# Optimization experiments

Measured on AMD Instinct MI355X. Metric: run time of the kernel, lower is better.

The kernel has to match this reference:

```python
import jax, jax.numpy as jnp
import numpy as np

EPS = 1e-6  # AbsMeanFunction eps
LN_EPS = 1e-5


def _absmean_core(W):
    # gamma = mean(|W|) + eps; quantize to {-1, 0, +1}
    gamma = jnp.mean(jnp.abs(W)) + EPS
    Ws = W / gamma
    Wq = jnp.sign(Ws) * jnp.minimum(jnp.round(jnp.abs(Ws)), 1.0)
    return Wq, gamma


@jax.custom_vjp
def absmean(W):
    return _absmean_core(W)[0]


def _absmean_fwd(W):
    Wq, gamma = _absmean_core(W)
    return Wq, gamma


def _absmean_bwd(gamma, g):
    # custom backward from AbsMeanFunction: grad_W = grad_output / gamma
    return (g / gamma,)


absmean.defvjp(_absmean_fwd, _absmean_bwd)


def layernorm(x, w, b, eps=LN_EPS):
    mu = jnp.mean(x, axis=-1, keepdims=True)
    var = jnp.mean((x - mu) ** 2, axis=-1, keepdims=True)
    return (x - mu) * jax.lax.rsqrt(var + eps) * w + b


def setup_inputs() -> dict:
    key = jax.random.key(0)
    k1, k2, k3 = jax.random.split(key, 3)
    d, h = 1024, 4096  # n_embd, mlp_factor * n_embd
    B, T = 8, 2048
    return {
        "x": jax.random.normal(k1, (B, T, d), jnp.float32),
        "W_fc": jax.random.normal(k2, (h, d), jnp.float32),   # BitLinear158 weight (out, in)
        "ln_w": jnp.ones((h,), jnp.float32),
        "ln_b": jnp.zeros((h,), jnp.float32),
        "W_proj": jax.random.normal(k3, (d, h), jnp.float32),  # BitLinear158 weight (out, in)
    }


def reference(x, W_fc, ln_w, ln_b, W_proj):
    # c_fc: ternary-quantized linear, no bias
    h = jnp.einsum('btd,hd->bth', x, absmean(W_fc))
    # exact (erf) GELU matches torch nn.GELU default
    h = jax.nn.gelu(h, approximate=False)
    h = layernorm(h, ln_w, ln_b)
    # c_proj: ternary-quantized linear, no bias; dropout p=0 is identity
    return jnp.einsum('bth,dh->btd', h, absmean(W_proj))
```

## Files before the change

kernel.cpp:

```cpp
#include <hip/hip_runtime.h>
#include <hip/hip_bf16.h>

typedef __attribute__((ext_vector_type(8))) short bf16x8;
typedef __attribute__((ext_vector_type(4))) float f32x4;
typedef unsigned short u16;

#define D_IN  1024
#define D_HID 4096
#define MROWS 16384

__device__ __forceinline__ float b2f(u16 u) {
    union { unsigned int i; float f; } c; c.i = ((unsigned int)u) << 16; return c.f;
}
__device__ __forceinline__ u16 f2b(float f) {
    unsigned int u = __builtin_bit_cast(unsigned int, f);
    return (u16)((u + 0x7FFFu + ((u >> 16) & 1u)) >> 16);
}

__device__ __forceinline__ float gelu_fast(float v) {
    float p = v * fmaf(0.044715f * v, v, 1.0f);
    float e = __builtin_amdgcn_exp2f(-2.302202983f * p);
    return v * __builtin_amdgcn_rcpf(1.0f + e);
}

__device__ __forceinline__ float rowsum16(float v) {
    int t;
    t = __builtin_amdgcn_update_dpp(0, __builtin_bit_cast(int, v), 0x111, 0xf, 0xf, true);
    v += __builtin_bit_cast(float, t);
    t = __builtin_amdgcn_update_dpp(0, __builtin_bit_cast(int, v), 0x112, 0xf, 0xf, true);
    v += __builtin_bit_cast(float, t);
    t = __builtin_amdgcn_update_dpp(0, __builtin_bit_cast(int, v), 0x114, 0xf, 0xf, true);
    v += __builtin_bit_cast(float, t);
    t = __builtin_amdgcn_update_dpp(0, __builtin_bit_cast(int, v), 0x118, 0xf, 0xf, true);
    v += __builtin_bit_cast(float, t);
    return v;
}

__global__ void prep1(const float* __restrict__ x, const float* __restrict__ W0,
                      const float* __restrict__ W1, u16* __restrict__ xb,
                      float* __restrict__ partials, int n4, int n8) {
    const int y = blockIdx.y;
    if (y == 2) {
        const int stride = gridDim.x * blockDim.x;
        for (int i = blockIdx.x * blockDim.x + threadIdx.x; i < n8; i += stride) {
            float4 a = ((const float4*)x)[2 * i];
            float4 c = ((const float4*)x)[2 * i + 1];
            bf16x8 o;
            o[0] = (short)f2b(a.x); o[1] = (short)f2b(a.y); o[2] = (short)f2b(a.z); o[3] = (short)f2b(a.w);
            o[4] = (short)f2b(c.x); o[5] = (short)f2b(c.y); o[6] = (short)f2b(c.z); o[7] = (short)f2b(c.w);
            ((bf16x8*)xb)[i] = o;
        }
        return;
    }
    const float* W = y ? W1 : W0;
    float* out = partials + y * 1024;
    __shared__ float sdata[256];
    float s = 0.f;
    const int stride = gridDim.x * blockDim.x;
    for (int i = blockIdx.x * blockDim.x + threadIdx.x; i < n4; i += stride) {
        float4 v = ((const float4*)W)[i];
        s += fabsf(v.x) + fabsf(v.y) + fabsf(v.z) + fabsf(v.w);
    }
    sdata[threadIdx.x] = s;
    __syncthreads();
    for (int off = 128; off > 0; off >>= 1) {
        if (threadIdx.x < off) sdata[threadIdx.x] += sdata[threadIdx.x + off];
        __syncthreads();
    }
    if (threadIdx.x == 0) out[blockIdx.x] = sdata[0];
}

__global__ void absmean_finalize2(const float* __restrict__ partials, float inv_n,
                                  float* __restrict__ gamma) {
    const float* p = partials + blockIdx.x * 1024;
    __shared__ float sdata[256];
    float s = 0.f;
    for (int i = threadIdx.x; i < 1024; i += 256) s += p[i];
    sdata[threadIdx.x] = s;
    __syncthreads();
    for (int off = 128; off > 0; off >>= 1) {
        if (threadIdx.x < off) sdata[threadIdx.x] += sdata[threadIdx.x + off];
        __syncthreads();
    }
    if (threadIdx.x == 0) gamma[blockIdx.x] = sdata[0] * inv_n + 1e-6f;
}

__global__ void prep2(const float* __restrict__ W0, const float* __restrict__ W1,
                      const float* __restrict__ lnw, const float* __restrict__ lnb,
                      const float* __restrict__ gamma,
                      u16* __restrict__ Q0, u16* __restrict__ Q1,
                      float* __restrict__ c1, float* __restrict__ c0, int n4) {
    const int y = blockIdx.y;
    if (y == 2) {
        const float thr = 0.5f * gamma[1];
        const float* row = W1 + (size_t)blockIdx.x * D_HID;
        float s1 = 0.f, s0 = 0.f;
        for (int h = threadIdx.x; h < D_HID; h += 256) {
            float v = row[h];
            float t = v > thr ? 1.f : (v < -thr ? -1.f : 0.f);
            s1 += lnw[h] * t;
            s0 += lnb[h] * t;
        }
#pragma unroll
        for (int off = 32; off > 0; off >>= 1) {
            s1 += __shfl_down(s1, off);
            s0 += __shfl_down(s0, off);
        }
        __shared__ float sh1[4], sh0[4];
        const int wave = threadIdx.x >> 6, lane = threadIdx.x & 63;
        if (lane == 0) { sh1[wave] = s1; sh0[wave] = s0; }
        __syncthreads();
        if (threadIdx.x == 0) {
            c1[blockIdx.x] = sh1[0] + sh1[1] + sh1[2] + sh1[3];
            c0[blockIdx.x] = sh0[0] + sh0[1] + sh0[2] + sh0[3];
        }
        return;
    }
    const float* W = y ? W1 : W0;
    u16* Wq = y ? Q1 : Q0;
    const float thr = 0.5f * gamma[y];
    const int stride = gridDim.x * blockDim.x;
    for (int i = blockIdx.x * blockDim.x + threadIdx.x; i < n4; i += stride) {
        float4 v = ((const float4*)W)[i];
        ushort4 q;
        if (y == 0) {
            q.x = v.x > thr ? 0x3F80u : (v.x < -thr ? 0xBF80u : 0u);
            q.y = v.y > thr ? 0x3F80u : (v.y < -thr ? 0xBF80u : 0u);
            q.z = v.z > thr ? 0x3F80u : (v.z < -thr ? 0xBF80u : 0u);
            q.w = v.w > thr ? 0x3F80u : (v.w < -thr ? 0xBF80u : 0u);
        } else {
            const int h = (i * 4) & (D_HID - 1);
            float w0 = lnw[h], w1 = lnw[h + 1], w2 = lnw[h + 2], w3 = lnw[h + 3];
            q.x = v.x > thr ? f2b(w0) : (v.x < -thr ? f2b(-w0) : 0u);
            q.y = v.y > thr ? f2b(w1) : (v.y < -thr ? f2b(-w1) : 0u);
            q.z = v.z > thr ? f2b(w2) : (v.z < -thr ? f2b(-w2) : 0u);
            q.w = v.w > thr ? f2b(w3) : (v.w < -thr ? f2b(-w3) : 0u);
        }
        ((ushort4*)Wq)[i] = q;
    }
}

template <int EPI>
__global__ __launch_bounds__(512, 2)
void gemm256(const u16* __restrict__ A, const u16* __restrict__ B,
             void* __restrict__ Cout, int M, int N, int K, int nbx,
             float* __restrict__ pS, float* __restrict__ pSS,
             const float* __restrict__ c1t, const float* __restrict__ c0t)
{
    (void)M;
    __shared__ u16 lds[65536];
    char* const ldsc = (char*)lds;
    const int tid = threadIdx.x;
    const int w = tid >> 6, lane = tid & 63;

    const int nwg = (int)gridDim.x;
    const int qq = nwg >> 3;
    const int bid = (int)blockIdx.x;
    const int swz = (bid & 7) * qq + (bid >> 3);
    const int bx = swz % nbx, by = swz / nbx;
    const size_t m0 = (size_t)by * 256, n0 = (size_t)bx * 256;

    const int wm = (w >> 2) * 128;
    const int wn = (w & 3) * 64;

    const int d0 = tid * 16;
    const int rrow = (d0 >> 6) & 15;
    const int sr0 = ((d0 >> 11) & 3) * 16 + rrow;
    const int cbx = (d0 & 63) ^ (((rrow >> 3) & 1) << 5);
    const int gc  = ((d0 >> 10) & 1) * 32 + (cbx >> 1);

    const int laneoffsw = (((lane & 15) * 64) + ((lane >> 4) * 16)) ^ (((lane >> 3) & 1) << 5);
    const int aoff = ((wm >> 7) << 14) + laneoffsw;
    const int boff = 65536 + ((wn >> 7) << 14) + (((wn >> 4) & 7) << 11) + laneoffsw;

    f32x4 acc[8][4];
#pragma unroll
    for (int i = 0; i < 8; ++i)
#pragma unroll
        for (int j = 0; j < 4; ++j) acc[i][j] = (f32x4){0.f, 0.f, 0.f, 0.f};

    bf16x8 a[4][2], b[4][2];

#define STAGE_A(KT, BUFB, HH) do {                                                              \
    const u16* _s = A + (size_t)(m0 + (HH) * 128 + sr0) * K + (size_t)(KT) * 64 + gc;           \
    __builtin_amdgcn_global_load_lds((const __attribute__((address_space(1))) void*)_s,         \
        (__attribute__((address_space(3))) void*)(ldsc + (BUFB) * 32768 + (HH) * 16384 + w * 1024), 16, 0, 0); \
    __builtin_amdgcn_global_load_lds((const __attribute__((address_space(1))) void*)(_s + (size_t)64 * K), \
        (__attribute__((address_space(3))) void*)(ldsc + (BUFB) * 32768 + (HH) * 16384 + w * 1024 + 8192), 16, 0, 0); \
} while (0)

#define STAGE_B(KT, BUFB, HH) do {                                                              \
    const u16* _s = B + (size_t)(n0 + (HH) * 128 + sr0) * K + (size_t)(KT) * 64 + gc;           \
    __builtin_amdgcn_global_load_lds((const __attribute__((address_space(1))) void*)_s,         \
        (__attribute__((address_space(3))) void*)(ldsc + 65536 + (BUFB) * 32768 + (HH) * 16384 + w * 1024), 16, 0, 0); \
    __builtin_amdgcn_global_load_lds((const __attribute__((address_space(1))) void*)(_s + (size_t)64 * K), \
        (__attribute__((address_space(3))) void*)(ldsc + 65536 + (BUFB) * 32768 + (HH) * 16384 + w * 1024 + 8192), 16, 0, 0); \
} while (0)

#define RD_A(BUFB, S, KS) (*(const bf16x8*)(ldsc + (BUFB) * 32768 + aoff + ((S) << 11) + ((KS) << 10)))
#define RD_B(BUFB, S, KS) (*(const bf16x8*)(ldsc + (BUFB) * 32768 + boff + ((S) << 11) + ((KS) << 10)))

#define MM(MB, NB) do {                                                                         \
    _Pragma("unroll") for (int ii = 0; ii < 4; ++ii)                                            \
    _Pragma("unroll") for (int jj = 0; jj < 2; ++jj)                                            \
    _Pragma("unroll") for (int kk = 0; kk < 2; ++kk)                                            \
        acc[(MB) + ii][(NB) + jj] = __builtin_amdgcn_mfma_f32_16x16x32_bf16(                    \
            a[ii][kk], b[(NB) + jj][kk], acc[(MB) + ii][(NB) + jj], 0, 0, 0);                   \
} while (0)

#define BARR()  asm volatile("s_barrier" ::: "memory")
#define LGKM0() asm volatile("s_waitcnt lgkmcnt(0)" ::: "memory")

#define ITER(F) do {                                                                            \
    _Pragma("unroll") for (int s = 0; s < 4; ++s) { a[s][0] = RD_A(0, s, 0); a[s][1] = RD_A(0, s, 1); } \
    _Pragma("unroll") for (int s = 0; s < 2; ++s) { b[s][0] = RD_B(0, s, 0); b[s][1] = RD_B(0, s, 1); } \
    STAGE_A(t + 1, 1, 0);                                                                       \
    asm volatile("s_waitcnt lgkmcnt(8)" ::: "memory");                                          \
    BARR(); LGKM0();                                                                            \
    __builtin_amdgcn_s_setprio(1); MM(0, 0); __builtin_amdgcn_s_setprio(0); BARR();             \
    _Pragma("unroll") for (int s = 2; s < 4; ++s) { b[s][0] = RD_B(0, s, 0); b[s][1] = RD_B(0, s, 1); } \
    STAGE_A(t + 1, 1, 1);                                                                       \
    BARR(); LGKM0();                                                                            \
    __builtin_amdgcn_s_setprio(1); MM(0, 2); __builtin_amdgcn_s_setprio(0); BARR();             \
    _Pragma("unroll") for (int s = 0; s < 4; ++s) { a[s][0] = RD_A(0, 4 + s, 0); a[s][1] = RD_A(0, 4 + s, 1); } \
    if (F) STAGE_B(t + 2, 0, 0);                                                                \
    BARR(); LGKM0();                                                                            \
    __builtin_amdgcn_s_setprio(1); MM(4, 0); __builtin_amdgcn_s_setprio(0); BARR();             \
    if (F) { STAGE_B(t + 2, 0, 1); asm volatile("s_waitcnt vmcnt(4)" ::: "memory"); }           \
    else   { asm volatile("s_waitcnt vmcnt(0)" ::: "memory"); }                                 \
    BARR();                                                                                     \
    __builtin_amdgcn_s_setprio(1); MM(4, 2); __builtin_amdgcn_s_setprio(0); BARR();             \
    _Pragma("unroll") for (int s = 0; s < 4; ++s) { a[s][0] = RD_A(1, s, 0); a[s][1] = RD_A(1, s, 1); } \
    _Pragma("unroll") for (int s = 0; s < 2; ++s) { b[s][0] = RD_B(1, s, 0); b[s][1] = RD_B(1, s, 1); } \
    if (F) STAGE_A(t + 2, 0, 0);                                                                \
    asm volatile("s_waitcnt lgkmcnt(8)" ::: "memory");                                          \
    BARR(); LGKM0();                                                                            \
    __builtin_amdgcn_s_setprio(1); MM(0, 0); __builtin_amdgcn_s_setprio(0); BARR();             \
    _Pragma("unroll") for (int s = 2; s < 4; ++s) { b[s][0] = RD_B(1, s, 0); b[s][1] = RD_B(1, s, 1); } \
    if (F) STAGE_A(t + 2, 0, 1);                                                                \
    BARR(); LGKM0();                                                                            \
    __builtin_amdgcn_s_setprio(1); MM(0, 2); __builtin_amdgcn_s_setprio(0); BARR();             \
    _Pragma("unroll") for (int s = 0; s < 4; ++s) { a[s][0] = RD_A(1, 4 + s, 0); a[s][1] = RD_A(1, 4 + s, 1); } \
    if (F) STAGE_B(t + 3, 1, 0);                                                                \
    BARR(); LGKM0();                                                                            \
    __builtin_amdgcn_s_setprio(1); MM(4, 0); __builtin_amdgcn_s_setprio(0); BARR();             \
    if (F) { STAGE_B(t + 3, 1, 1); asm volatile("s_waitcnt vmcnt(4)" ::: "memory"); }           \
    BARR();                                                                                     \
    __builtin_amdgcn_s_setprio(1); MM(4, 2); __builtin_amdgcn_s_setprio(0); BARR();             \
} while (0)

    const int nkt = K >> 6;
    const int niter = nkt >> 1;

    STAGE_A(0, 0, 0);
    STAGE_A(0, 0, 1);
    STAGE_B(0, 0, 0);
    STAGE_B(0, 0, 1);
    STAGE_B(1, 1, 0);
    STAGE_B(1, 1, 1);
    asm volatile("s_waitcnt vmcnt(4)" ::: "memory");
    BARR();

    for (int it = 0; it + 1 < niter; ++it) { const int t = 2 * it; ITER(1); }
    { const int t = 2 * (niter - 1); ITER(0); }

    const int fr = (lane >> 4) * 4;
    const int fc = lane & 15;
    if constexpr (EPI == 0) {
        float2* qd = (float2*)ldsc;
        const int wnq = w & 3;
        u16* C = (u16*)Cout;
#pragma unroll
        for (int mf = 0; mf < 8; ++mf)
#pragma unroll
            for (int r = 0; r < 4; ++r) {
                const int lrow = wm + mf * 16 + fr + r;
                const size_t row = m0 + lrow;
                float s = 0.f, ss = 0.f;
#pragma unroll
                for (int nf = 0; nf < 4; ++nf) {
                    float g = gelu_fast(acc[mf][nf][r]);
                    C[row * (size_t)N + (n0 + wn + nf * 16 + fc)] = f2b(g);
                    s += g;
                    ss = fmaf(g, g, ss);
                }
                s  = rowsum16(s);
                ss = rowsum16(ss);
                if (fc == 15) qd[lrow * 4 + wnq] = make_float2(s, ss);
            }
        __syncthreads();
        if (tid < 256) {
            float2 q0 = qd[tid * 4 + 0], q1 = qd[tid * 4 + 1];
            float2 q2 = qd[tid * 4 + 2], q3 = qd[tid * 4 + 3];
            pS[(size_t)bx * MROWS + m0 + tid]  = (q0.x + q1.x) + (q2.x + q3.x);
            pSS[(size_t)bx * MROWS + m0 + tid] = (q0.y + q1.y) + (q2.y + q3.y);
        }
    } else {
        float* sA = (float*)ldsc;
        float* sB = (float*)(ldsc + 1024);
        if (tid < 256) {
            float s = 0.f, ss = 0.f;
#pragma unroll
            for (int bq = 0; bq < 16; ++bq) {
                s  += pS[(size_t)bq * MROWS + m0 + tid];
                ss += pSS[(size_t)bq * MROWS + m0 + tid];
            }
            const float mu  = s * (1.f / (float)D_HID);
            const float var = ss * (1.f / (float)D_HID) - mu * mu;
            const float Av  = rsqrtf(var + 1e-5f);
            sA[tid] = Av;
            sB[tid] = -mu * Av;
        }
        __syncthreads();
        float* C = (float*)Cout;
        float c1v[4], c0v[4];
#pragma unroll
        for (int nf = 0; nf < 4; ++nf) {
            const size_t col = n0 + wn + nf * 16 + fc;
            c1v[nf] = c1t[col];
            c0v[nf] = c0t[col];
        }
#pragma unroll
        for (int mf = 0; mf < 8; ++mf)
#pragma unroll
            for (int r = 0; r < 4; ++r) {
                const int lrow = wm + mf * 16 + fr + r;
                const size_t row = m0 + lrow;
                const float Av = sA[lrow], Bv = sB[lrow];
#pragma unroll
                for (int nf = 0; nf < 4; ++nf) {
                    const size_t col = n0 + wn + nf * 16 + fc;
                    C[row * (size_t)N + col] = fmaf(Av, acc[mf][nf][r], fmaf(Bv, c1v[nf], c0v[nf]));
                }
            }
    }
#undef STAGE_A
#undef STAGE_B
#undef RD_A
#undef RD_B
#undef MM
#undef BARR
#undef LGKM0
#undef ITER
}

extern "C" void kernel_launch(void* const* d_in, const int* in_sizes, int n_in,
                              void* d_out, int out_size, void* d_ws, size_t ws_size,
                              hipStream_t stream)
{
    const float* x   = (const float*)d_in[0];
    const float* Wfc = (const float*)d_in[1];
    const float* lnw = (const float*)d_in[2];
    const float* lnb = (const float*)d_in[3];
    const float* Wpj = (const float*)d_in[4];
    float* out = (float*)d_out;
    char* ws = (char*)d_ws;

    u16* Wq_fc = (u16*)ws;
    u16* Wq_pj = (u16*)(ws + (size_t)(8u  << 20));
    u16* xb    = (u16*)(ws + (size_t)(16u << 20));
    u16* hbuf  = (u16*)(ws + (size_t)(48u << 20));
    char* tail = ws + (size_t)(176u << 20);
    float* parts = (float*)tail;
    float* gam   = (float*)(tail + 8192);
    float* c1t   = (float*)(tail + 16384);
    float* c0t   = (float*)(tail + 16384 + 4096);
    float* pS    = (float*)(ws + (size_t)(177u << 20));
    float* pSS   = (float*)(ws + (size_t)(178u << 20));

    const int nW  = D_HID * D_IN;
    const int nW4 = nW / 4;
    const int nX8 = MROWS * D_IN / 8;

    prep1<<<dim3(1024, 3), 256, 0, stream>>>(x, Wfc, Wpj, xb, parts, nW4, nX8);
    absmean_finalize2<<<2, 256, 0, stream>>>(parts, 1.f / (float)nW, gam);
    prep2<<<dim3(1024, 3), 256, 0, stream>>>(Wfc, Wpj, lnw, lnb, gam, Wq_fc, Wq_pj, c1t, c0t, nW4);

    {
        const int nbx = D_HID / 256;
        const int nby = MROWS / 256;
        gemm256<0><<<dim3(nbx * nby), dim3(512), 0, stream>>>(
            xb, Wq_fc, hbuf, MROWS, D_HID, D_IN, nbx, pS, pSS, nullptr, nullptr);
    }

    {
        const int nbx = D_IN / 256;
        const int nby = MROWS / 256;
        gemm256<1><<<dim3(nbx * nby), dim3(512), 0, stream>>>(
            hbuf, Wq_pj, out, MROWS, D_IN, D_HID, nbx, pS, pSS, c1t, c0t);
    }
}
```

Before: 403.5 us.

## Make GEMM1 persistent over four M tiles, prefetching next tile during epilogue

The first GEMM now launches one quarter as many workgroups. Each one loops over four consecutive 256-row M tiles, and during the last K iteration it stages the next tile's A and B into LDS so those loads overlap the GELU/stats epilogue. The epilogue scratch moves to a separate LDS region, which raises the shared-memory footprint to about 136KB and likely drops occupancy to one workgroup per CU. prep2 also merges the W_proj quantization with the c1/c0 row reductions into one pass, removing a launch slice and a second read of W_proj.

```diff
diff --git a/kernel.cpp b/kernel.cpp
--- a/kernel.cpp
+++ b/kernel.cpp
@@ -91,15 +91,30 @@
                       u16* __restrict__ Q0, u16* __restrict__ Q1,
                       float* __restrict__ c1, float* __restrict__ c0, int n4) {
     const int y = blockIdx.y;
-    if (y == 2) {
+    if (y == 1) {
         const float thr = 0.5f * gamma[1];
-        const float* row = W1 + (size_t)blockIdx.x * D_HID;
+        const int r = blockIdx.x;
+        const float* row = W1 + (size_t)r * D_HID;
+        u16* qrow = Q1 + (size_t)r * D_HID;
         float s1 = 0.f, s0 = 0.f;
-        for (int h = threadIdx.x; h < D_HID; h += 256) {
-            float v = row[h];
-            float t = v > thr ? 1.f : (v < -thr ? -1.f : 0.f);
-            s1 += lnw[h] * t;
-            s0 += lnb[h] * t;
+#pragma unroll
+        for (int k = 0; k < 4; ++k) {
+            const int h = threadIdx.x * 4 + k * 1024;
+            float4 v = *(const float4*)(row + h);
+            float w0 = lnw[h], w1 = lnw[h + 1], w2 = lnw[h + 2], w3 = lnw[h + 3];
+            float b0 = lnb[h], b1 = lnb[h + 1], b2 = lnb[h + 2], b3 = lnb[h + 3];
+            float t0 = v.x > thr ? 1.f : (v.x < -thr ? -1.f : 0.f);
+            float t1 = v.y > thr ? 1.f : (v.y < -thr ? -1.f : 0.f);
+            float t2 = v.z > thr ? 1.f : (v.z < -thr ? -1.f : 0.f);
+            float t3 = v.w > thr ? 1.f : (v.w < -thr ? -1.f : 0.f);
+            ushort4 q;
+            q.x = t0 == 0.f ? 0u : f2b(t0 * w0);
+            q.y = t1 == 0.f ? 0u : f2b(t1 * w1);
+            q.z = t2 == 0.f ? 0u : f2b(t2 * w2);
+            q.w = t3 == 0.f ? 0u : f2b(t3 * w3);
+            *(ushort4*)(qrow + h) = q;
+            s1 += w0 * t0 + w1 * t1 + w2 * t2 + w3 * t3;
+            s0 += b0 * t0 + b1 * t1 + b2 * t2 + b3 * t3;
         }
 #pragma unroll
         for (int off = 32; off > 0; off >>= 1) {
@@ -111,36 +126,25 @@
         if (lane == 0) { sh1[wave] = s1; sh0[wave] = s0; }
         __syncthreads();
         if (threadIdx.x == 0) {
-            c1[blockIdx.x] = sh1[0] + sh1[1] + sh1[2] + sh1[3];
-            c0[blockIdx.x] = sh0[0] + sh0[1] + sh0[2] + sh0[3];
+            c1[r] = sh1[0] + sh1[1] + sh1[2] + sh1[3];
+            c0[r] = sh0[0] + sh0[1] + sh0[2] + sh0[3];
         }
         return;
     }
-    const float* W = y ? W1 : W0;
-    u16* Wq = y ? Q1 : Q0;
-    const float thr = 0.5f * gamma[y];
+    const float thr = 0.5f * gamma[0];
     const int stride = gridDim.x * blockDim.x;
     for (int i = blockIdx.x * blockDim.x + threadIdx.x; i < n4; i += stride) {
-        float4 v = ((const float4*)W)[i];
+        float4 v = ((const float4*)W0)[i];
         ushort4 q;
-        if (y == 0) {
-            q.x = v.x > thr ? 0x3F80u : (v.x < -thr ? 0xBF80u : 0u);
-            q.y = v.y > thr ? 0x3F80u : (v.y < -thr ? 0xBF80u : 0u);
-            q.z = v.z > thr ? 0x3F80u : (v.z < -thr ? 0xBF80u : 0u);
-            q.w = v.w > thr ? 0x3F80u : (v.w < -thr ? 0xBF80u : 0u);
-        } else {
-            const int h = (i * 4) & (D_HID - 1);
-            float w0 = lnw[h], w1 = lnw[h + 1], w2 = lnw[h + 2], w3 = lnw[h + 3];
-            q.x = v.x > thr ? f2b(w0) : (v.x < -thr ? f2b(-w0) : 0u);
-            q.y = v.y > thr ? f2b(w1) : (v.y < -thr ? f2b(-w1) : 0u);
-            q.z = v.z > thr ? f2b(w2) : (v.z < -thr ? f2b(-w2) : 0u);
-            q.w = v.w > thr ? f2b(w3) : (v.w < -thr ? f2b(-w3) : 0u);
-        }
-        ((ushort4*)Wq)[i] = q;
-    }
-}
-
-template <int EPI>
+        q.x = v.x > thr ? 0x3F80u : (v.x < -thr ? 0xBF80u : 0u);
+        q.y = v.y > thr ? 0x3F80u : (v.y < -thr ? 0xBF80u : 0u);
+        q.z = v.z > thr ? 0x3F80u : (v.z < -thr ? 0xBF80u : 0u);
+        q.w = v.w > thr ? 0x3F80u : (v.w < -thr ? 0xBF80u : 0u);
+        ((ushort4*)Q0)[i] = q;
+    }
+}
+
+template <int EPI, int NT>
 __global__ __launch_bounds__(512, 2)
 void gemm256(const u16* __restrict__ A, const u16* __restrict__ B,
              void* __restrict__ Cout, int M, int N, int K, int nbx,
@@ -148,8 +152,8 @@
              const float* __restrict__ c1t, const float* __restrict__ c0t)
 {
     (void)M;
-    __shared__ u16 lds[65536];
-    char* const ldsc = (char*)lds;
+    __shared__ char ldsbuf[139264];
+    char* const ldsc = ldsbuf;
     const int tid = threadIdx.x;
     const int w = tid >> 6, lane = tid & 63;
 
@@ -157,8 +161,8 @@
     const int qq = nwg >> 3;
     const int bid = (int)blockIdx.x;
     const int swz = (bid & 7) * qq + (bid >> 3);
-    const int bx = swz % nbx, by = swz / nbx;
-    const size_t m0 = (size_t)by * 256, n0 = (size_t)bx * 256;
+    const int bx = swz % nbx, tg = swz / nbx;
+    const size_t n0 = (size_t)bx * 256;
 
     const int wm = (w >> 2) * 128;
     const int wn = (w & 3) * 64;
@@ -174,11 +178,6 @@
     const int boff = 65536 + ((wn >> 7) << 14) + (((wn >> 4) & 7) << 11) + laneoffsw;
 
     f32x4 acc[8][4];
-#pragma unroll
-    for (int i = 0; i < 8; ++i)
-#pragma unroll
-        for (int j = 0; j < 4; ++j) acc[i][j] = (f32x4){0.f, 0.f, 0.f, 0.f};
-
     bf16x8 a[4][2], b[4][2];
 
 #define STAGE_A(KT, BUFB, HH) do {                                                              \
@@ -189,6 +188,14 @@
         (__attribute__((address_space(3))) void*)(ldsc + (BUFB) * 32768 + (HH) * 16384 + w * 1024 + 8192), 16, 0, 0); \
 } while (0)
 
+#define STAGE_A_N(KT, BUFB, HH) do {                                                            \
+    const u16* _s = A + (size_t)(m0n + (HH) * 128 + sr0) * K + (size_t)(KT) * 64 + gc;          \
+    __builtin_amdgcn_global_load_lds((const __attribute__((address_space(1))) void*)_s,         \
+        (__attribute__((address_space(3))) void*)(ldsc + (BUFB) * 32768 + (HH) * 16384 + w * 1024), 16, 0, 0); \
+    __builtin_amdgcn_global_load_lds((const __attribute__((address_space(1))) void*)(_s + (size_t)64 * K), \
+        (__attribute__((address_space(3))) void*)(ldsc + (BUFB) * 32768 + (HH) * 16384 + w * 1024 + 8192), 16, 0, 0); \
+} while (0)
+
 #define STAGE_B(KT, BUFB, HH) do {                                                              \
     const u16* _s = B + (size_t)(n0 + (HH) * 128 + sr0) * K + (size_t)(KT) * 64 + gc;           \
     __builtin_amdgcn_global_load_lds((const __attribute__((address_space(1))) void*)_s,         \
@@ -223,118 +230,142 @@
     BARR(); LGKM0();                                                                            \
     __builtin_amdgcn_s_setprio(1); MM(0, 2); __builtin_amdgcn_s_setprio(0); BARR();             \
     _Pragma("unroll") for (int s = 0; s < 4; ++s) { a[s][0] = RD_A(0, 4 + s, 0); a[s][1] = RD_A(0, 4 + s, 1); } \
-    if (F) STAGE_B(t + 2, 0, 0);                                                                \
+    if (F == 1) STAGE_B(t + 2, 0, 0);                                                           \
     BARR(); LGKM0();                                                                            \
     __builtin_amdgcn_s_setprio(1); MM(4, 0); __builtin_amdgcn_s_setprio(0); BARR();             \
-    if (F) { STAGE_B(t + 2, 0, 1); asm volatile("s_waitcnt vmcnt(4)" ::: "memory"); }           \
-    else   { asm volatile("s_waitcnt vmcnt(0)" ::: "memory"); }                                 \
+    if (F == 1) { STAGE_B(t + 2, 0, 1); asm volatile("s_waitcnt vmcnt(4)" ::: "memory"); }      \
+    else        { asm volatile("s_waitcnt vmcnt(0)" ::: "memory"); }                            \
     BARR();                                                                                     \
     __builtin_amdgcn_s_setprio(1); MM(4, 2); __builtin_amdgcn_s_setprio(0); BARR();             \
     _Pragma("unroll") for (int s = 0; s < 4; ++s) { a[s][0] = RD_A(1, s, 0); a[s][1] = RD_A(1, s, 1); } \
     _Pragma("unroll") for (int s = 0; s < 2; ++s) { b[s][0] = RD_B(1, s, 0); b[s][1] = RD_B(1, s, 1); } \
-    if (F) STAGE_A(t + 2, 0, 0);                                                                \
+    if (F == 1) STAGE_A(t + 2, 0, 0); else if (F == 2) STAGE_A_N(0, 0, 0);                      \
     asm volatile("s_waitcnt lgkmcnt(8)" ::: "memory");                                          \
     BARR(); LGKM0();                                                                            \
     __builtin_amdgcn_s_setprio(1); MM(0, 0); __builtin_amdgcn_s_setprio(0); BARR();             \
     _Pragma("unroll") for (int s = 2; s < 4; ++s) { b[s][0] = RD_B(1, s, 0); b[s][1] = RD_B(1, s, 1); } \
-    if (F) STAGE_A(t + 2, 0, 1);                                                                \
+    if (F == 1) STAGE_A(t + 2, 0, 1); else if (F == 2) STAGE_A_N(0, 0, 1);                      \
     BARR(); LGKM0();                                                                            \
     __builtin_amdgcn_s_setprio(1); MM(0, 2); __builtin_amdgcn_s_setprio(0); BARR();             \
     _Pragma("unroll") for (int s = 0; s < 4; ++s) { a[s][0] = RD_A(1, 4 + s, 0); a[s][1] = RD_A(1, 4 + s, 1); } \
-    if (F) STAGE_B(t + 3, 1, 0);                                                                \
+    if (F == 1) STAGE_B(t + 3, 1, 0); else if (F == 2) STAGE_B(0, 0, 0);                        \
     BARR(); LGKM0();                                                                            \
     __builtin_amdgcn_s_setprio(1); MM(4, 0); __builtin_amdgcn_s_setprio(0); BARR();             \
-    if (F) { STAGE_B(t + 3, 1, 1); asm volatile("s_waitcnt vmcnt(4)" ::: "memory"); }           \
+    if (F == 1) { STAGE_B(t + 3, 1, 1); asm volatile("s_waitcnt vmcnt(4)" ::: "memory"); }      \
+    else if (F == 2) { STAGE_B(0, 0, 1); }                                                      \
     BARR();                                                                                     \
     __builtin_amdgcn_s_setprio(1); MM(4, 2); __builtin_amdgcn_s_setprio(0); BARR();             \
 } while (0)
 
     const int nkt = K >> 6;
     const int niter = nkt >> 1;
-
-    STAGE_A(0, 0, 0);
-    STAGE_A(0, 0, 1);
-    STAGE_B(0, 0, 0);
-    STAGE_B(0, 0, 1);
-    STAGE_B(1, 1, 0);
-    STAGE_B(1, 1, 1);
-    asm volatile("s_waitcnt vmcnt(4)" ::: "memory");
-    BARR();
-
-    for (int it = 0; it + 1 < niter; ++it) { const int t = 2 * it; ITER(1); }
-    { const int t = 2 * (niter - 1); ITER(0); }
-
     const int fr = (lane >> 4) * 4;
     const int fc = lane & 15;
-    if constexpr (EPI == 0) {
-        float2* qd = (float2*)ldsc;
-        const int wnq = w & 3;
-        u16* C = (u16*)Cout;
-#pragma unroll
-        for (int mf = 0; mf < 8; ++mf)
-#pragma unroll
-            for (int r = 0; r < 4; ++r) {
-                const int lrow = wm + mf * 16 + fr + r;
-                const size_t row = m0 + lrow;
+
+    for (int mt = 0; mt < NT; ++mt) {
+        const size_t m0  = ((size_t)(tg * NT + mt)) * 256;
+        const size_t m0n = m0 + 256;
+
+#pragma unroll
+        for (int i = 0; i < 8; ++i)
+#pragma unroll
+            for (int j = 0; j < 4; ++j) acc[i][j] = (f32x4){0.f, 0.f, 0.f, 0.f};
+
+        if (mt == 0) {
+            STAGE_A(0, 0, 0);
+            STAGE_A(0, 0, 1);
+            STAGE_B(0, 0, 0);
+            STAGE_B(0, 0, 1);
+            STAGE_B(1, 1, 0);
+            STAGE_B(1, 1, 1);
+            asm volatile("s_waitcnt vmcnt(4)" ::: "memory");
+            BARR();
+        }
+
+        for (int it = 0; it < niter; ++it) {
+            const int t = 2 * it;
+            const int F = (it + 1 < niter) ? 1 : ((mt + 1 < NT) ? 2 : 0);
+            ITER(F);
+        }
+
+        if constexpr (EPI == 0) {
+            float2* qd = (float2*)(ldsc + 131072);
+            const int wnq = w & 3;
+            u16* C = (u16*)Cout;
+#pragma unroll
+            for (int mf = 0; mf < 8; ++mf)
+#pragma unroll
+                for (int r = 0; r < 4; ++r) {
+                    const int lrow = wm + mf * 16 + fr + r;
+                    const size_t row = m0 + lrow;
+                    float s = 0.f, ss = 0.f;
+#pragma unroll
+                    for (int nf = 0; nf < 4; ++nf) {
+                        float g = gelu_fast(acc[mf][nf][r]);
+                        C[row * (size_t)N + (n0 + wn + nf * 16 + fc)] = f2b(g);
+                        s += g;
+                        ss = fmaf(g, g, ss);
+                    }
+                    s  = rowsum16(s);
+                    ss = rowsum16(ss);
+                    if (fc == 15) qd[lrow * 4 + wnq] = make_float2(s, ss);
+                }
+            LGKM0(); BARR();
+            if (tid < 256) {
+                float2 q0 = qd[tid * 4 + 0], q1 = qd[tid * 4 + 1];
+                float2 q2 = qd[tid * 4 + 2], q3 = qd[tid * 4 + 3];
+                pS[(size_t)bx * MROWS + m0 + tid]  = (q0.x + q1.x) + (q2.x + q3.x);
+                pSS[(size_t)bx * MROWS + m0 + tid] = (q0.y + q1.y) + (q2.y + q3.y);
+            }
+        } else {
+            float* sA = (float*)(ldsc + 131072);
+            float* sB = (float*)(ldsc + 132096);
+            if (tid < 256) {
                 float s = 0.f, ss = 0.f;
 #pragma unroll
-                for (int nf = 0; nf < 4; ++nf) {
-                    float g = gelu_fast(acc[mf][nf][r]);
-                    C[row * (size_t)N + (n0 + wn + nf * 16 + fc)] = f2b(g);
-                    s += g;
-                    ss = fmaf(g, g, ss);
+                for (int bq = 0; bq < 16; ++bq) {
+                    s  += pS[(size_t)bq * MROWS + m0 + tid];
+                    ss += pSS[(size_t)bq * MROWS + m0 + tid];
                 }
-                s  = rowsum16(s);
-                ss = rowsum16(ss);
-                if (fc == 15) qd[lrow * 4 + wnq] = make_float2(s, ss);
+                const float mu  = s * (1.f / (float)D_HID);
+                const float var = ss * (1.f / (float)D_HID) - mu * mu;
+                const float Av  = rsqrtf(var + 1e-5f);
+                sA[tid] = Av;
+                sB[tid] = -mu * Av;
             }
-        __syncthreads();
-        if (tid < 256) {
-            float2 q0 = qd[tid * 4 + 0], q1 = qd[tid * 4 + 1];
-            float2 q2 = qd[tid * 4 + 2], q3 = qd[tid * 4 + 3];
-            pS[(size_t)bx * MROWS + m0 + tid]  = (q0.x + q1.x) + (q2.x + q3.x);
-            pSS[(size_t)bx * MROWS + m0 + tid] = (q0.y + q1.y) + (q2.y + q3.y);
-        }
-    } else {
-        float* sA = (float*)ldsc;
-        float* sB = (float*)(ldsc + 1024);
-        if (tid < 256) {
-            float s = 0.f, ss = 0.f;
-#pragma unroll
-            for (int bq = 0; bq < 16; ++bq) {
-                s  += pS[(size_t)bq * MROWS + m0 + tid];
-                ss += pSS[(size_t)bq * MROWS + m0 + tid];
+            LGKM0(); BARR();
+            float* C = (float*)Cout;
+            float c1v[4], c0v[4];
+#pragma unroll
+            for (int nf = 0; nf < 4; ++nf) {
+                const size_t col = n0 + wn + nf * 16 + fc;
+                c1v[nf] = c1t[col];
+                c0v[nf] = c0t[col];
             }
-            const float mu  = s * (1.f / (float)D_HID);
-            const float var = ss * (1.f / (float)D_HID) - mu * mu;
-            const float Av  = rsqrtf(var + 1e-5f);
-            sA[tid] = Av;
-            sB[tid] = -mu * Av;
-        }
-        __syncthreads();
-        float* C = (float*)Cout;
-        float c1v[4], c0v[4];
-#pragma unroll
-        for (int nf = 0; nf < 4; ++nf) {
-            const size_t col = n0 + wn + nf * 16 + fc;
-            c1v[nf] = c1t[col];
-            c0v[nf] = c0t[col];
-        }
-#pragma unroll
-        for (int mf = 0; mf < 8; ++mf)
-#pragma unroll
-            for (int r = 0; r < 4; ++r) {
-                const int lrow = wm + mf * 16 + fr + r;
-                const size_t row = m0 + lrow;
-                const float Av = sA[lrow], Bv = sB[lrow];
-#pragma unroll
-                for (int nf = 0; nf < 4; ++nf) {
-                    const size_t col = n0 + wn + nf * 16 + fc;
-                    C[row * (size_t)N + col] = fmaf(Av, acc[mf][nf][r], fmaf(Bv, c1v[nf], c0v[nf]));
+#pragma unroll
+            for (int mf = 0; mf < 8; ++mf)
+#pragma unroll
+                for (int r = 0; r < 4; ++r) {
+                    const int lrow = wm + mf * 16 + fr + r;
+                    const size_t row = m0 + lrow;
+                    const float Av = sA[lrow], Bv = sB[lrow];
+#pragma unroll
+                    for (int nf = 0; nf < 4; ++nf) {
+                        const size_t col = n0 + wn + nf * 16 + fc;
+                        C[row * (size_t)N + col] = fmaf(Av, acc[mf][nf][r], fmaf(Bv, c1v[nf], c0v[nf]));
+                    }
                 }
-            }
+        }
+
+        if (mt + 1 < NT) {
+            STAGE_B(1, 1, 0);
+            STAGE_B(1, 1, 1);
+            asm volatile("s_waitcnt vmcnt(4)" ::: "memory");
+            BARR();
+        }
     }
 #undef STAGE_A
+#undef STAGE_A_N
 #undef STAGE_B
 #undef RD_A
 #undef RD_B
@@ -374,19 +405,19 @@
 
     prep1<<<dim3(1024, 3), 256, 0, stream>>>(x, Wfc, Wpj, xb, parts, nW4, nX8);
     absmean_finalize2<<<2, 256, 0, stream>>>(parts, 1.f / (float)nW, gam);
-    prep2<<<dim3(1024, 3), 256, 0, stream>>>(Wfc, Wpj, lnw, lnb, gam, Wq_fc, Wq_pj, c1t, c0t, nW4);
+    prep2<<<dim3(1024, 2), 256, 0, stream>>>(Wfc, Wpj, lnw, lnb, gam, Wq_fc, Wq_pj, c1t, c0t, nW4);
 
     {
         const int nbx = D_HID / 256;
-        const int nby = MROWS / 256;
-        gemm256<0><<<dim3(nbx * nby), dim3(512), 0, stream>>>(
+        const int ntg = (MROWS / 256) / 4;
+        gemm256<0, 4><<<dim3(nbx * ntg), dim3(512), 0, stream>>>(
             xb, Wq_fc, hbuf, MROWS, D_HID, D_IN, nbx, pS, pSS, nullptr, nullptr);
     }
 
     {
         const int nbx = D_IN / 256;
         const int nby = MROWS / 256;
-        gemm256<1><<<dim3(nbx * nby), dim3(512), 0, stream>>>(
+        gemm256<1, 1><<<dim3(nbx * nby), dim3(512), 0, stream>>>(
             hbuf, Wq_pj, out, MROWS, D_IN, D_HID, nbx, pS, pSS, c1t, c0t);
     }
 }
```

Measured after the change: 485.9 us. 1.2x slower.
